# Performance work log

Hardware: AMD Instinct MI355X
Metric: run time of the kernel (lower is better)

## Reference

```python
import jax, jax.numpy as jnp
import numpy as np

NUM_HEADS = 16
CLAMP = 1e4


def setup_inputs() -> dict:
    key = jax.random.key(0)
    ks = jax.random.split(key, 8)
    B, Nq, Nkv, Cq, Ckv = 4, 2048, 2048, 1024, 768
    s_q = 1.0 / np.sqrt(Cq)
    s_kv = 1.0 / np.sqrt(Ckv)
    return {
        "query": jax.random.normal(ks[0], (B, Nq, Cq), jnp.float32),
        "key_value": jax.random.normal(ks[1], (B, Nkv, Ckv), jnp.float32),
        "Wq": jax.random.normal(ks[2], (Cq, Cq), jnp.float32) * s_q,
        "bq": jnp.zeros((Cq,), jnp.float32),
        "Wk": jax.random.normal(ks[3], (Ckv, Cq), jnp.float32) * s_kv,
        "bk": jnp.zeros((Cq,), jnp.float32),
        "Wv": jax.random.normal(ks[4], (Ckv, Cq), jnp.float32) * s_kv,
        "bv": jnp.zeros((Cq,), jnp.float32),
        "Wo": jax.random.normal(ks[5], (Cq, Cq), jnp.float32) * s_q,
        "bo": jnp.zeros((Cq,), jnp.float32),
    }


def reference(query, key_value, Wq, bq, Wk, bk, Wv, bv, Wo, bo):
    B, Nq, Cq = query.shape
    Nkv = key_value.shape[1]
    H = NUM_HEADS
    D = Cq // H
    scale = D ** (-0.5)

    # projections -> [B, H, N, D]
    q = (query @ Wq + bq).reshape(B, Nq, H, D).transpose(0, 2, 1, 3)
    k = (key_value @ Wk + bk).reshape(B, Nkv, H, D).transpose(0, 2, 1, 3)
    v = (key_value @ Wv + bv).reshape(B, Nkv, H, D).transpose(0, 2, 1, 3)

    # scores [B, H, Nq, Nkv] with clamp (mask=None path)
    attn = jnp.einsum("bhqd,bhkd->bhqk", q, k) * scale
    attn = jnp.clip(attn, -CLAMP, CLAMP)
    attn = jax.nn.softmax(attn, axis=-1)
    # NaN fallback: replace with uniform attention if any NaN present
    attn = jnp.where(jnp.any(jnp.isnan(attn)),
                     jnp.asarray(1.0 / Nkv, attn.dtype), attn)

    # weighted sum -> [B, Nq, Cq]
    x = jnp.einsum("bhqk,bhkd->bqhd", attn, v).reshape(B, Nq, Cq)
    return x @ Wo + bo
```

## Files before the change

### kernel.cpp

```cpp
#include <hip/hip_runtime.h>
#include <hip/hip_bf16.h>
#include <stdint.h>


typedef unsigned short u16;
typedef __attribute__((ext_vector_type(4))) short bf16x4;
typedef __attribute__((ext_vector_type(8))) short bf16x8;
typedef __attribute__((ext_vector_type(4))) float f32x4;
typedef __attribute__((ext_vector_type(16))) float f32x16;

__device__ __forceinline__ u16 f2bf(float x) {
  union { float f; uint32_t u; } c; c.f = x;
  uint32_t r = c.u + 0x7fffu + ((c.u >> 16) & 1u);
  return (u16)(r >> 16);
}

__device__ __forceinline__ uint32_t pkbf(float a, float b) {
#if __has_builtin(__builtin_amdgcn_cvt_pk_bf16_f32)
  typedef __attribute__((ext_vector_type(2))) __bf16 bf2;
  bf2 r = __builtin_amdgcn_cvt_pk_bf16_f32(a, b);
  return __builtin_bit_cast(uint32_t, r);
#else
  return (uint32_t)f2bf(a) | ((uint32_t)f2bf(b) << 16);
#endif
}

__device__ __forceinline__ void gld16(const void* g, void* l) {
  __builtin_amdgcn_global_load_lds(
      (const __attribute__((address_space(1))) void*)g,
      (__attribute__((address_space(3))) void*)l, 16, 0, 0);
}

__device__ __forceinline__ void cvt_body(const float* __restrict__ in,
                                         u16* __restrict__ out, int blk) {
  int i = (blk * 256 + threadIdx.x) * 8;
  float4 a = *(const float4*)(in + i);
  float4 b = *(const float4*)(in + i + 4);
  union { u16 u[8]; uint4 v; } o;
  o.u[0] = f2bf(a.x); o.u[1] = f2bf(a.y); o.u[2] = f2bf(a.z); o.u[3] = f2bf(a.w);
  o.u[4] = f2bf(b.x); o.u[5] = f2bf(b.y); o.u[6] = f2bf(b.z); o.u[7] = f2bf(b.w);
  *(uint4*)(out + i) = o.v;
}

__device__ __forceinline__ void transpose_body(const float* __restrict__ in,
                                               u16* __restrict__ out,
                                               int R, int C, int bx, int by) {
  __shared__ float tile[64][65];
  int c0 = bx * 64, r0 = by * 64;
  #pragma unroll
  for (int it = 0; it < 16; it++) {
    int idx = threadIdx.x + it * 256;
    int lr = idx >> 6, lc = idx & 63;
    tile[lr][lc] = in[(size_t)(r0 + lr) * C + c0 + lc];
  }
  __syncthreads();
  #pragma unroll
  for (int it = 0; it < 16; it++) {
    int idx = threadIdx.x + it * 256;
    int lc = idx >> 6, lr = idx & 63;
    out[(size_t)(c0 + lc) * R + r0 + lr] = f2bf(tile[lr][lc]);
  }
}

__global__ void prep_kernel(const float* __restrict__ query,
                            const float* __restrict__ key_value,
                            const float* __restrict__ Wq, const float* __restrict__ Wk,
                            const float* __restrict__ Wv, const float* __restrict__ Wo,
                            u16* qb, u16* kvb, u16* WqT, u16* WkT, u16* WvT, u16* WoT) {
  int blk = blockIdx.x;
  if (blk < 4096) { cvt_body(query, qb, blk); return; }
  if (blk < 7168) { cvt_body(key_value, kvb, blk - 4096); return; }
  if (blk < 7424) { int lo = blk - 7168; transpose_body(Wq, WqT, 1024, 1024, lo & 15, lo >> 4); return; }
  if (blk < 7616) { int lo = blk - 7424; transpose_body(Wk, WkT, 768, 1024, lo & 15, lo >> 4); return; }
  if (blk < 7808) { int lo = blk - 7616; transpose_body(Wv, WvT, 768, 1024, lo & 15, lo >> 4); return; }
  { int lo = blk - 7808; transpose_body(Wo, WoT, 1024, 1024, lo & 15, lo >> 4); return; }
}

template<int MODE>
__global__ __launch_bounds__(256, 2)
void gemm_bt(const u16* __restrict__ A, const u16* __restrict__ BT,
             const float* __restrict__ bias, void* __restrict__ Cout,
             int M, int N, int K, float scale) {
  __shared__ __align__(16) char smem[36864];
  const int tid = threadIdx.x;
  const int w = tid >> 6, l = tid & 63;
  const int lm = l & 15, lq = l >> 4;
  const int m0 = blockIdx.y * 128, n0 = blockIdx.x * 128;
  const int wr = w >> 1, wc = w & 1;
  f32x4 acc[4][4] = {};

  const u16* ap[4]; const u16* bp[4]; int ldA[4], ldB[4];
  #pragma unroll
  for (int it2 = 0; it2 < 4; it2++) {
    int s = it2 * 256 + tid;
    int row = s >> 3, cl = (s & 7) ^ (row & 7);
    ap[it2] = A + (size_t)(m0 + row) * K + cl * 8;
    bp[it2] = BT + (size_t)(n0 + row) * K + cl * 8;
    ldA[it2] = s * 16;
    ldB[it2] = 16384 + s * 16;
  }
  int abase[4], bbase[4];
  #pragma unroll
  for (int i = 0; i < 4; i++) {
    int m = wr * 64 + i * 16 + lm;
    abase[i] = m * 128 + ((lq ^ (m & 7)) << 4);
    int n = wc * 64 + i * 16 + lm;
    bbase[i] = 16384 + n * 128 + ((lq ^ (n & 7)) << 4);
  }

  for (int k0 = 0; k0 < K; k0 += 64) {
    #pragma unroll
    for (int it2 = 0; it2 < 4; it2++) {
      gld16(ap[it2], smem + ldA[it2]);
      gld16(bp[it2], smem + ldB[it2]);
      ap[it2] += 64; bp[it2] += 64;
    }
    __syncthreads();
    #pragma unroll
    for (int kk = 0; kk < 2; kk++) {
      bf16x8 af[4], bf[4];
      #pragma unroll
      for (int i = 0; i < 4; i++)
        af[i] = *(const bf16x8*)(smem + (abase[i] ^ (kk << 6)));
      #pragma unroll
      for (int j = 0; j < 4; j++)
        bf[j] = *(const bf16x8*)(smem + (bbase[j] ^ (kk << 6)));
      #pragma unroll
      for (int i = 0; i < 4; i++)
        #pragma unroll
        for (int j = 0; j < 4; j++) {
          if (MODE == 1)
            acc[i][j] = __builtin_amdgcn_mfma_f32_16x16x32_bf16(bf[j], af[i], acc[i][j], 0, 0, 0);
          else
            acc[i][j] = __builtin_amdgcn_mfma_f32_16x16x32_bf16(af[i], bf[j], acc[i][j], 0, 0, 0);
        }
    }
    __syncthreads();
  }

  if (MODE == 0) {
    #pragma unroll
    for (int j = 0; j < 4; j++) {
      int gn = n0 + wc * 64 + j * 16 + lm;
      float bi = bias[gn];
      #pragma unroll
      for (int i = 0; i < 4; i++) {
        int gm = m0 + wr * 64 + i * 16 + lq * 4;
        #pragma unroll
        for (int r = 0; r < 4; r++)
          ((float*)Cout)[(size_t)(gm + r) * N + gn] = (acc[i][j][r] + bi) * scale;
      }
    }
    return;
  }

  u16* etile = (u16*)(smem + w * 9216);
  const int xr = l >> 3, cc = (l & 7) ^ xr;

  if (MODE == 1) {
    #pragma unroll
    for (int j = 0; j < 4; j++) {
      float4 b4 = *(const float4*)&bias[n0 + wc * 64 + j * 16 + lq * 4];
      #pragma unroll
      for (int i = 0; i < 4; i++) {
        uint2 pkd;
        pkd.x = pkbf((acc[i][j][0] + b4.x) * scale, (acc[i][j][1] + b4.y) * scale);
        pkd.y = pkbf((acc[i][j][2] + b4.z) * scale, (acc[i][j][3] + b4.w) * scale);
        *(uint2*)&etile[(i * 16 + lm) * 72 + j * 16 + lq * 4] = pkd;
      }
    }
    u16* gbase = (u16*)Cout + (size_t)(m0 + wr * 64) * N + n0 + wc * 64;
    #pragma unroll
    for (int co = 0; co < 8; co++) {
      int ml = co * 8 + xr;
      uint4 d = *(const uint4*)&etile[ml * 72 + cc * 8];
      *(uint4*)&gbase[(size_t)ml * N + cc * 8] = d;
    }
  } else {
    #pragma unroll
    for (int j = 0; j < 4; j++) {
      float bi = bias[n0 + wc * 64 + j * 16 + lm];
      #pragma unroll
      for (int i = 0; i < 4; i++) {
        uint2 pkd;
        pkd.x = pkbf(acc[i][j][0] + bi, acc[i][j][1] + bi);
        pkd.y = pkbf(acc[i][j][2] + bi, acc[i][j][3] + bi);
        *(uint2*)&etile[(j * 16 + lm) * 72 + i * 16 + lq * 4] = pkd;
      }
    }
    const int bb = m0 >> 11, mloc = (m0 & 2047) + wr * 64;
    u16* gbase = (u16*)Cout + ((size_t)bb * N + n0 + wc * 64) * 2048 + mloc;
    #pragma unroll
    for (int co = 0; co < 8; co++) {
      int dl = co * 8 + xr;
      uint4 d = *(const uint4*)&etile[dl * 72 + cc * 8];
      *(uint4*)&gbase[(size_t)dl * 2048 + cc * 8] = d;
    }
  }
}

__global__ __launch_bounds__(256, 3)
void attn_kernel(const u16* __restrict__ Q, const u16* __restrict__ Kb,
                 const u16* __restrict__ Vt, u16* __restrict__ X) {
  __shared__ __align__(16) char smem[32768];
  const int tid = threadIdx.x, w = tid >> 6, l = tid & 63;
  const int l31 = l & 31, h5 = l >> 5;
  const int bh = blockIdx.x, b = bh >> 4, h = bh & 15;
  const int q0 = blockIdx.y * 128 + w * 32;
  const int rx = l31 & 7;

  const u16* Kg = Kb + (size_t)b * 2048 * 1024 + h * 64;
  const u16* Vg = Vt + (size_t)bh * 64 * 2048;

  const u16 *kp0, *kp1, *vp0, *vp1;
  {
    int s = tid, r = s >> 3, c = (s & 7) ^ (r & 7);
    kp0 = Kg + (size_t)r * 1024 + c * 8;
    vp0 = Vg + (size_t)r * 2048 + c * 8;
    s = 256 + tid; r = s >> 3; c = (s & 7) ^ (r & 7);
    kp1 = Kg + (size_t)r * 1024 + c * 8;
    vp1 = Vg + (size_t)r * 2048 + c * 8;
  }
  const int kd0 = tid * 16, kd1 = (256 + tid) * 16;

  bf16x8 qf[4];
  {
    const u16* qp = Q + ((size_t)(b * 2048 + q0 + l31)) * 1024 + h * 64 + h5 * 8;
    #pragma unroll
    for (int t = 0; t < 4; t++) qf[t] = *(const bf16x8*)(qp + t * 16);
  }

  const int kvb_ = (l31 << 7) | ((rx ^ h5) << 4);
  const int vbase_ = 16384 | (l31 << 7) | (rx << 4) | (h5 << 3);

  f32x16 xacc[2] = {};
  f32x4 ls4 = {0.f, 0.f, 0.f, 0.f};
  const f32x16 KZ = {};

  gld16(kp0, smem + kd0); gld16(kp1, smem + kd1);
  gld16(vp0, smem + 16384 + kd0); gld16(vp1, smem + 16384 + kd1);
  kp0 += 65536; kp1 += 65536; vp0 += 64; vp1 += 64;
  __syncthreads();

  for (int it = 0; it < 32; it++) {
    const int cur = it & 1;
    if (it < 31) {
      const int nb = (cur ^ 1) << 13;
      gld16(kp0, smem + nb + kd0); gld16(kp1, smem + nb + kd1);
      gld16(vp0, smem + 16384 + nb + kd0); gld16(vp1, smem + 16384 + nb + kd1);
      kp0 += 65536; kp1 += 65536; vp0 += 64; vp1 += 64;
    }
    #pragma unroll
    for (int sub = 0; sub < 2; sub++) {
      const int km = (cur << 13) | (sub << 12);
      bf16x8 kf = *(const bf16x8*)(smem + (kvb_ ^ km));
      f32x16 st = __builtin_amdgcn_mfma_f32_32x32x16_bf16(kf, qf[0], KZ, 0, 0, 0);
      #pragma unroll
      for (int t = 1; t < 4; t++) {
        kf = *(const bf16x8*)(smem + (kvb_ ^ (km | (t << 5))));
        st = __builtin_amdgcn_mfma_f32_32x32x16_bf16(kf, qf[t], st, 0, 0, 0);
      }
      float p[16];
      #pragma unroll
      for (int r = 0; r < 16; r++) p[r] = __builtin_amdgcn_exp2f(st[r]);
      #pragma unroll
      for (int u = 0; u < 4; u++)
        ls4[u] += (p[4 * u] + p[4 * u + 1]) + (p[4 * u + 2] + p[4 * u + 3]);
      uint32_t pk[8];
      #pragma unroll
      for (int qd = 0; qd < 8; qd++) pk[qd] = pkbf(p[2 * qd], p[2 * qd + 1]);
      #pragma unroll
      for (int c2 = 0; c2 < 2; c2++) {
        union { uint32_t d[4]; bf16x8 v; } pf;
        pf.d[0] = pk[4 * c2 + 0]; pf.d[1] = pk[4 * c2 + 1];
        pf.d[2] = pk[4 * c2 + 2]; pf.d[3] = pk[4 * c2 + 3];
        #pragma unroll
        for (int dt = 0; dt < 2; dt++) {
          const int vm = (cur << 13) | (dt << 12) | (((sub << 2) | (c2 << 1)) << 4);
          union { bf16x4 hlf[2]; bf16x8 v; } vf;
          vf.hlf[0] = *(const bf16x4*)(smem + (vbase_ ^ vm));
          vf.hlf[1] = *(const bf16x4*)(smem + (vbase_ ^ (vm | 16)));
          xacc[dt] = __builtin_amdgcn_mfma_f32_32x32x16_bf16(vf.v, pf.v, xacc[dt], 0, 0, 0);
        }
      }
    }
    __syncthreads();
  }

  float lsum = (ls4[0] + ls4[1]) + (ls4[2] + ls4[3]);
  const float inv = 1.0f / (lsum + __shfl_xor(lsum, 32));
  u16* xp = X + ((size_t)(b * 2048 + q0 + l31)) * 1024 + h * 64;
  #pragma unroll
  for (int dt = 0; dt < 2; dt++)
    #pragma unroll
    for (int g = 0; g < 4; g++) {
      const int d0 = dt * 32 + g * 8 + h5 * 4;
      uint2 o;
      o.x = pkbf(xacc[dt][4 * g + 0] * inv, xacc[dt][4 * g + 1] * inv);
      o.y = pkbf(xacc[dt][4 * g + 2] * inv, xacc[dt][4 * g + 3] * inv);
      *(uint2*)(xp + d0) = o;
    }
}

extern "C" void kernel_launch(void* const* d_in, const int* in_sizes, int n_in,
                              void* d_out, int out_size, void* d_ws, size_t ws_size,
                              hipStream_t stream) {
  const float* query     = (const float*)d_in[0];
  const float* key_value = (const float*)d_in[1];
  const float* Wq = (const float*)d_in[2];
  const float* bq = (const float*)d_in[3];
  const float* Wk = (const float*)d_in[4];
  const float* bk = (const float*)d_in[5];
  const float* Wv = (const float*)d_in[6];
  const float* bv = (const float*)d_in[7];
  const float* Wo = (const float*)d_in[8];
  const float* bo = (const float*)d_in[9];
  float* out = (float*)d_out;

  char* ws = (char*)d_ws;
  size_t off = 0;
  auto alloc = [&](size_t bytes) -> void* {
    void* p = ws + off; off += (bytes + 255) & ~(size_t)255; return p;
  };
  u16* qb  = (u16*)alloc((size_t)8192 * 1024 * 2);
  u16* kvb = (u16*)alloc((size_t)8192 * 768 * 2);
  u16* WqT = (u16*)alloc((size_t)1024 * 1024 * 2);
  u16* WkT = (u16*)alloc((size_t)1024 * 768 * 2);
  u16* WvT = (u16*)alloc((size_t)1024 * 768 * 2);
  u16* WoT = (u16*)alloc((size_t)1024 * 1024 * 2);
  u16* Qb  = (u16*)alloc((size_t)8192 * 1024 * 2);
  u16* Kbf = (u16*)alloc((size_t)8192 * 1024 * 2);
  u16* Vt  = (u16*)alloc((size_t)8192 * 1024 * 2);
  u16* Xb  = (u16*)alloc((size_t)8192 * 1024 * 2);

  prep_kernel<<<8064, 256, 0, stream>>>(query, key_value, Wq, Wk, Wv, Wo,
                                        qb, kvb, WqT, WkT, WvT, WoT);

  const float qscale = 0.125f * 1.4426950408889634f;
  gemm_bt<1><<<dim3(8, 64), 256, 0, stream>>>(qb, WqT, bq, Qb, 8192, 1024, 1024, qscale);
  gemm_bt<1><<<dim3(8, 64), 256, 0, stream>>>(kvb, WkT, bk, Kbf, 8192, 1024, 768, 1.0f);
  gemm_bt<2><<<dim3(8, 64), 256, 0, stream>>>(kvb, WvT, bv, Vt, 8192, 1024, 768, 1.0f);

  attn_kernel<<<dim3(64, 16), 256, 0, stream>>>(Qb, Kbf, Vt, Xb);

  gemm_bt<0><<<dim3(8, 64), 256, 0, stream>>>(Xb, WoT, bo, out, 8192, 1024, 1024, 1.0f);
}
```

Baseline: 312.1 us.

## Merge QKV projection GEMMs into one launch and retile V layout for attention

```diff
diff --git a/kernel.cpp b/kernel.cpp
--- a/kernel.cpp
+++ b/kernel.cpp
@@ -76,19 +76,11 @@
   { int lo = blk - 7808; transpose_body(Wo, WoT, 1024, 1024, lo & 15, lo >> 4); return; }
 }
 
-template<int MODE>
-__global__ __launch_bounds__(256, 2)
-void gemm_bt(const u16* __restrict__ A, const u16* __restrict__ BT,
-             const float* __restrict__ bias, void* __restrict__ Cout,
-             int M, int N, int K, float scale) {
-  __shared__ __align__(16) char smem[36864];
-  const int tid = threadIdx.x;
-  const int w = tid >> 6, l = tid & 63;
-  const int lm = l & 15, lq = l >> 4;
-  const int m0 = blockIdx.y * 128, n0 = blockIdx.x * 128;
-  const int wr = w >> 1, wc = w & 1;
-  f32x4 acc[4][4] = {};
-
+template<bool SWAP>
+__device__ __forceinline__ void gemm_kloop(const u16* __restrict__ A,
+                                           const u16* __restrict__ BT,
+                                           int K, char* smem, f32x4 (&acc)[4][4],
+                                           int m0, int n0, int tid) {
   const u16* ap[4]; const u16* bp[4]; int ldA[4], ldB[4];
   #pragma unroll
   for (int it2 = 0; it2 < 4; it2++) {
@@ -99,6 +91,9 @@
     ldA[it2] = s * 16;
     ldB[it2] = 16384 + s * 16;
   }
+  const int w = tid >> 6, l = tid & 63;
+  const int lm = l & 15, lq = l >> 4;
+  const int wr = w >> 1, wc = w & 1;
   int abase[4], bbase[4];
   #pragma unroll
   for (int i = 0; i < 4; i++) {
@@ -107,7 +102,6 @@
     int n = wc * 64 + i * 16 + lm;
     bbase[i] = 16384 + n * 128 + ((lq ^ (n & 7)) << 4);
   }
-
   for (int k0 = 0; k0 < K; k0 += 64) {
     #pragma unroll
     for (int it2 = 0; it2 < 4; it2++) {
@@ -129,7 +123,7 @@
       for (int i = 0; i < 4; i++)
         #pragma unroll
         for (int j = 0; j < 4; j++) {
-          if (MODE == 1)
+          if (SWAP)
             acc[i][j] = __builtin_amdgcn_mfma_f32_16x16x32_bf16(bf[j], af[i], acc[i][j], 0, 0, 0);
           else
             acc[i][j] = __builtin_amdgcn_mfma_f32_16x16x32_bf16(af[i], bf[j], acc[i][j], 0, 0, 0);
@@ -137,27 +131,36 @@
     }
     __syncthreads();
   }
-
-  if (MODE == 0) {
-    #pragma unroll
-    for (int j = 0; j < 4; j++) {
-      int gn = n0 + wc * 64 + j * 16 + lm;
-      float bi = bias[gn];
-      #pragma unroll
-      for (int i = 0; i < 4; i++) {
-        int gm = m0 + wr * 64 + i * 16 + lq * 4;
-        #pragma unroll
-        for (int r = 0; r < 4; r++)
-          ((float*)Cout)[(size_t)(gm + r) * N + gn] = (acc[i][j][r] + bi) * scale;
-      }
-    }
-    return;
-  }
+}
+
+__global__ __launch_bounds__(256, 2)
+void gemm_qkv(const u16* __restrict__ qb, const u16* __restrict__ kvb,
+              const u16* __restrict__ WqT, const u16* __restrict__ WkT,
+              const u16* __restrict__ WvT,
+              const float* __restrict__ bq, const float* __restrict__ bk,
+              const float* __restrict__ bv,
+              u16* __restrict__ Qb, u16* __restrict__ Kbf, u16* __restrict__ Vt,
+              float qscale) {
+  extern __shared__ __align__(16) char smem[];
+  const int tid = threadIdx.x;
+  const int w = tid >> 6, l = tid & 63;
+  const int lm = l & 15, lq = l >> 4;
+  const int m0 = blockIdx.y * 128, n0 = blockIdx.x * 128;
+  const int wr = w >> 1, wc = w & 1;
+  const int z = blockIdx.z;
+  f32x4 acc[4][4] = {};
 
   u16* etile = (u16*)(smem + w * 9216);
   const int xr = l >> 3, cc = (l & 7) ^ xr;
 
-  if (MODE == 1) {
+  if (z < 2) {
+    const u16* A = (z == 0) ? qb : kvb;
+    const u16* BT = (z == 0) ? WqT : WkT;
+    const float* bias = (z == 0) ? bq : bk;
+    u16* out = (z == 0) ? Qb : Kbf;
+    const float scale = (z == 0) ? qscale : 1.0f;
+    const int K = (z == 0) ? 1024 : 768;
+    gemm_kloop<true>(A, BT, K, smem, acc, m0, n0, tid);
     #pragma unroll
     for (int j = 0; j < 4; j++) {
       float4 b4 = *(const float4*)&bias[n0 + wc * 64 + j * 16 + lq * 4];
@@ -169,17 +172,18 @@
         *(uint2*)&etile[(i * 16 + lm) * 72 + j * 16 + lq * 4] = pkd;
       }
     }
-    u16* gbase = (u16*)Cout + (size_t)(m0 + wr * 64) * N + n0 + wc * 64;
+    u16* gbase = out + (size_t)(m0 + wr * 64) * 1024 + n0 + wc * 64;
     #pragma unroll
     for (int co = 0; co < 8; co++) {
       int ml = co * 8 + xr;
       uint4 d = *(const uint4*)&etile[ml * 72 + cc * 8];
-      *(uint4*)&gbase[(size_t)ml * N + cc * 8] = d;
+      *(uint4*)&gbase[(size_t)ml * 1024 + cc * 8] = d;
     }
   } else {
+    gemm_kloop<false>(kvb, WvT, 768, smem, acc, m0, n0, tid);
     #pragma unroll
     for (int j = 0; j < 4; j++) {
-      float bi = bias[n0 + wc * 64 + j * 16 + lm];
+      float bi = bv[n0 + wc * 64 + j * 16 + lm];
       #pragma unroll
       for (int i = 0; i < 4; i++) {
         uint2 pkd;
@@ -189,12 +193,40 @@
       }
     }
     const int bb = m0 >> 11, mloc = (m0 & 2047) + wr * 64;
-    u16* gbase = (u16*)Cout + ((size_t)bb * N + n0 + wc * 64) * 2048 + mloc;
+    u16* gbase = Vt + ((size_t)bb * 1024 + n0 + wc * 64) * 2048 + mloc;
+    const int kvA = (cc >> 1) * 16 + (cc & 1) * 4;
     #pragma unroll
     for (int co = 0; co < 8; co++) {
       int dl = co * 8 + xr;
-      uint4 d = *(const uint4*)&etile[dl * 72 + cc * 8];
+      uint2 dA = *(const uint2*)&etile[dl * 72 + kvA];
+      uint2 dB = *(const uint2*)&etile[dl * 72 + kvA + 8];
+      uint4 d = {dA.x, dA.y, dB.x, dB.y};
       *(uint4*)&gbase[(size_t)dl * 2048 + cc * 8] = d;
+    }
+  }
+}
+
+__global__ __launch_bounds__(256, 2)
+void gemm_o(const u16* __restrict__ A, const u16* __restrict__ BT,
+            const float* __restrict__ bias, float* __restrict__ Cout) {
+  __shared__ __align__(16) char smem[32768];
+  const int tid = threadIdx.x;
+  const int w = tid >> 6, l = tid & 63;
+  const int lm = l & 15, lq = l >> 4;
+  const int m0 = blockIdx.y * 128, n0 = blockIdx.x * 128;
+  const int wr = w >> 1, wc = w & 1;
+  f32x4 acc[4][4] = {};
+  gemm_kloop<false>(A, BT, 1024, smem, acc, m0, n0, tid);
+  #pragma unroll
+  for (int j = 0; j < 4; j++) {
+    int gn = n0 + wc * 64 + j * 16 + lm;
+    float bi = bias[gn];
+    #pragma unroll
+    for (int i = 0; i < 4; i++) {
+      int gm = m0 + wr * 64 + i * 16 + lq * 4;
+      #pragma unroll
+      for (int r = 0; r < 4; r++)
+        Cout[(size_t)(gm + r) * 1024 + gn] = acc[i][j][r] + bi;
     }
   }
 }
@@ -230,8 +262,8 @@
     for (int t = 0; t < 4; t++) qf[t] = *(const bf16x8*)(qp + t * 16);
   }
 
-  const int kvb_ = (l31 << 7) | ((rx ^ h5) << 4);
-  const int vbase_ = 16384 | (l31 << 7) | (rx << 4) | (h5 << 3);
+  const int kvb2 = (l31 << 7) | ((rx ^ h5) << 4);
+  const int vb2 = 16384 | (l31 << 7) | ((rx ^ h5) << 4);
 
   f32x16 xacc[2] = {};
   f32x4 ls4 = {0.f, 0.f, 0.f, 0.f};
@@ -242,50 +274,57 @@
   kp0 += 65536; kp1 += 65536; vp0 += 64; vp1 += 64;
   __syncthreads();
 
-  for (int it = 0; it < 32; it++) {
-    const int cur = it & 1;
-    if (it < 31) {
-      const int nb = (cur ^ 1) << 13;
-      gld16(kp0, smem + nb + kd0); gld16(kp1, smem + nb + kd1);
-      gld16(vp0, smem + 16384 + nb + kd0); gld16(vp1, smem + 16384 + nb + kd1);
-      kp0 += 65536; kp1 += 65536; vp0 += 64; vp1 += 64;
-    }
-    #pragma unroll
-    for (int sub = 0; sub < 2; sub++) {
-      const int km = (cur << 13) | (sub << 12);
-      bf16x8 kf = *(const bf16x8*)(smem + (kvb_ ^ km));
-      f32x16 st = __builtin_amdgcn_mfma_f32_32x32x16_bf16(kf, qf[0], KZ, 0, 0, 0);
-      #pragma unroll
-      for (int t = 1; t < 4; t++) {
-        kf = *(const bf16x8*)(smem + (kvb_ ^ (km | (t << 5))));
-        st = __builtin_amdgcn_mfma_f32_32x32x16_bf16(kf, qf[t], st, 0, 0, 0);
-      }
-      float p[16];
-      #pragma unroll
-      for (int r = 0; r < 16; r++) p[r] = __builtin_amdgcn_exp2f(st[r]);
-      #pragma unroll
-      for (int u = 0; u < 4; u++)
-        ls4[u] += (p[4 * u] + p[4 * u + 1]) + (p[4 * u + 2] + p[4 * u + 3]);
-      uint32_t pk[8];
-      #pragma unroll
-      for (int qd = 0; qd < 8; qd++) pk[qd] = pkbf(p[2 * qd], p[2 * qd + 1]);
-      #pragma unroll
-      for (int c2 = 0; c2 < 2; c2++) {
-        union { uint32_t d[4]; bf16x8 v; } pf;
-        pf.d[0] = pk[4 * c2 + 0]; pf.d[1] = pk[4 * c2 + 1];
-        pf.d[2] = pk[4 * c2 + 2]; pf.d[3] = pk[4 * c2 + 3];
-        #pragma unroll
-        for (int dt = 0; dt < 2; dt++) {
-          const int vm = (cur << 13) | (dt << 12) | (((sub << 2) | (c2 << 1)) << 4);
-          union { bf16x4 hlf[2]; bf16x8 v; } vf;
-          vf.hlf[0] = *(const bf16x4*)(smem + (vbase_ ^ vm));
-          vf.hlf[1] = *(const bf16x4*)(smem + (vbase_ ^ (vm | 16)));
-          xacc[dt] = __builtin_amdgcn_mfma_f32_32x32x16_bf16(vf.v, pf.v, xacc[dt], 0, 0, 0);
-        }
-      }
-    }
-    __syncthreads();
-  }
+#define ATTN_STEP(CUR, DOPREF)                                                  \
+  {                                                                             \
+    if (DOPREF) {                                                               \
+      const int nb = ((CUR) ^ 1) << 13;                                         \
+      gld16(kp0, smem + nb + kd0); gld16(kp1, smem + nb + kd1);                 \
+      gld16(vp0, smem + 16384 + nb + kd0); gld16(vp1, smem + 16384 + nb + kd1); \
+      kp0 += 65536; kp1 += 65536; vp0 += 64; vp1 += 64;                         \
+    }                                                                           \
+    _Pragma("unroll")                                                           \
+    for (int sub = 0; sub < 2; sub++) {                                         \
+      const int km = ((CUR) << 13) | (sub << 12);                               \
+      bf16x8 kf = *(const bf16x8*)(smem + (kvb2 ^ km));                         \
+      f32x16 st = __builtin_amdgcn_mfma_f32_32x32x16_bf16(kf, qf[0], KZ, 0, 0, 0); \
+      _Pragma("unroll")                                                         \
+      for (int t = 1; t < 4; t++) {                                             \
+        kf = *(const bf16x8*)(smem + (kvb2 ^ (km | (t << 5))));                 \
+        st = __builtin_amdgcn_mfma_f32_32x32x16_bf16(kf, qf[t], st, 0, 0, 0);   \
+      }                                                                         \
+      float p[16];                                                              \
+      _Pragma("unroll")                                                         \
+      for (int r = 0; r < 16; r++) p[r] = __builtin_amdgcn_exp2f(st[r]);        \
+      _Pragma("unroll")                                                         \
+      for (int u = 0; u < 4; u++)                                               \
+        ls4[u] += (p[4 * u] + p[4 * u + 1]) + (p[4 * u + 2] + p[4 * u + 3]);    \
+      uint32_t pk[8];                                                           \
+      _Pragma("unroll")                                                         \
+      for (int qd = 0; qd < 8; qd++) pk[qd] = pkbf(p[2 * qd], p[2 * qd + 1]);   \
+      _Pragma("unroll")                                                         \
+      for (int c2 = 0; c2 < 2; c2++) {                                          \
+        union { uint32_t d[4]; bf16x8 v; } pf;                                  \
+        pf.d[0] = pk[4 * c2 + 0]; pf.d[1] = pk[4 * c2 + 1];                     \
+        pf.d[2] = pk[4 * c2 + 2]; pf.d[3] = pk[4 * c2 + 3];                     \
+        const int vx = ((sub << 2) | (c2 << 1)) << 4;                           \
+        _Pragma("unroll")                                                       \
+        for (int dt = 0; dt < 2; dt++) {                                        \
+          bf16x8 vf = *(const bf16x8*)(smem +                                   \
+              (vb2 ^ (((CUR) << 13) | (dt << 12) | vx)));                       \
+          xacc[dt] = __builtin_amdgcn_mfma_f32_32x32x16_bf16(vf, pf.v, xacc[dt], 0, 0, 0); \
+        }                                                                       \
+      }                                                                         \
+    }                                                                           \
+    __syncthreads();                                                            \
+  }
+
+  for (int itp = 0; itp < 15; itp++) {
+    ATTN_STEP(0, true)
+    ATTN_STEP(1, true)
+  }
+  ATTN_STEP(0, true)
+  ATTN_STEP(1, false)
+#undef ATTN_STEP
 
   float lsum = (ls4[0] + ls4[1]) + (ls4[2] + ls4[3]);
   const float inv = 1.0f / (lsum + __shfl_xor(lsum, 32));
@@ -337,11 +376,10 @@
                                         qb, kvb, WqT, WkT, WvT, WoT);
 
   const float qscale = 0.125f * 1.4426950408889634f;
-  gemm_bt<1><<<dim3(8, 64), 256, 0, stream>>>(qb, WqT, bq, Qb, 8192, 1024, 1024, qscale);
-  gemm_bt<1><<<dim3(8, 64), 256, 0, stream>>>(kvb, WkT, bk, Kbf, 8192, 1024, 768, 1.0f);
-  gemm_bt<2><<<dim3(8, 64), 256, 0, stream>>>(kvb, WvT, bv, Vt, 8192, 1024, 768, 1.0f);
+  gemm_qkv<<<dim3(8, 64, 3), 256, 36864, stream>>>(qb, kvb, WqT, WkT, WvT,
+                                                   bq, bk, bv, Qb, Kbf, Vt, qscale);
 
   attn_kernel<<<dim3(64, 16), 256, 0, stream>>>(Qb, Kbf, Vt, Xb);
 
-  gemm_bt<0><<<dim3(8, 64), 256, 0, stream>>>(Xb, WoT, bo, out, 8192, 1024, 1024, 1.0f);
-}
+  gemm_o<<<dim3(8, 64), 256, 0, stream>>>(Xb, WoT, bo, out);
+}
```

Result: faster. 293.1 us (-6.1%).
